# Optimization experiments

Hardware: AMD Instinct MI355X
Metric: run time of the kernel (lower is better)

Reference implementation:

```python
import jax, jax.numpy as jnp
import numpy as np

N_NODES = 100000
N_EDGES = 1600000
D_IN, D_HID, D_OUT = 128, 128, 64


def setup_inputs() -> dict:
    key = jax.random.key(0)
    ks = jax.random.split(key, 8)
    x = jax.random.normal(ks[0], (N_NODES, D_IN), dtype=jnp.float32)
    edge_index = jax.random.randint(ks[1], (2, N_EDGES), 0, N_NODES, dtype=jnp.int64)
    def glorot(k, fan_in, fan_out):
        s = jnp.sqrt(6.0 / (fan_in + fan_out))
        return jax.random.uniform(k, (fan_in, fan_out), jnp.float32, -s, s)
    return {
        "x": x,
        "edge_index": edge_index,
        "W1": glorot(ks[2], D_IN, D_HID), "b1": jnp.zeros((D_HID,), jnp.float32),
        "W2": glorot(ks[3], D_HID, D_HID), "b2": jnp.zeros((D_HID,), jnp.float32),
        "W3": glorot(ks[4], D_HID, D_OUT), "b3": jnp.zeros((D_OUT,), jnp.float32),
    }


def _gcn_norm(edge_index, n_nodes):
    # add self-loops, compute symmetric normalization D^-1/2 A D^-1/2
    loop = jnp.arange(n_nodes, dtype=edge_index.dtype)
    src = jnp.concatenate([edge_index[0], loop])  # message source
    dst = jnp.concatenate([edge_index[1], loop])  # aggregation target
    deg = jax.ops.segment_sum(jnp.ones_like(dst, dtype=jnp.float32), dst,
                              num_segments=n_nodes)
    dinv = jnp.where(deg > 0, jax.lax.rsqrt(deg), 0.0)
    norm = dinv[src] * dinv[dst]  # [E + N]
    return src, dst, norm


def _gcn_conv(x, W, b, src, dst, norm, n_nodes):
    xw = x @ W                                # dense transform [N, F_out]
    msg = xw[src] * norm[:, None]             # gather + scale   [E+N, F_out]
    out = jax.ops.segment_sum(msg, dst, num_segments=n_nodes)  # scatter-add
    return out + b


def reference(x, edge_index, W1, b1, W2, b2, W3, b3):
    n = x.shape[0]
    src, dst, norm = _gcn_norm(edge_index, n)  # cached=True: same norm reused
    h = jax.nn.relu(_gcn_conv(x, W1, b1, src, dst, norm, n))
    h = jax.nn.relu(_gcn_conv(h, W2, b2, src, dst, norm, n))
    return _gcn_conv(h, W3, b3, src, dst, norm, n)
```

## Files before the change

### kernel.cpp

```cpp
#include <hip/hip_runtime.h>
#include <hip/hip_fp16.h>


#define NN 100000
#define NE 1600000
#define TT (NE + NN)
#define BSH 9
#define NBUCK ((NN + 511) / 512)
#define EPB1 8192
#define NPB1 ((TT + EPB1 - 1) / EPB1)
#define SLOT 12288

typedef _Float16 f16x8 __attribute__((ext_vector_type(8)));
typedef float f32x4 __attribute__((ext_vector_type(4)));


__global__ __launch_bounds__(256) void wt_conv_all(const float* __restrict__ W1,
                                                   const float* __restrict__ W2,
                                                   const float* __restrict__ W3,
                                                   _Float16* __restrict__ Wt1,
                                                   _Float16* __restrict__ Wt2,
                                                   _Float16* __restrict__ Wt3,
                                                   int* __restrict__ gcursor,
                                                   int* __restrict__ rowptr) {
    int idx = blockIdx.x * 256 + threadIdx.x;
    if (idx < 16384) {
        Wt1[(idx % 128) * 128 + idx / 128] = (_Float16)W1[idx];
    } else if (idx < 32768) {
        int i = idx - 16384;
        Wt2[(i % 128) * 128 + i / 128] = (_Float16)W2[i];
    } else if (idx < 40960) {
        int i = idx - 32768;
        Wt3[(i % 64) * 128 + i / 64] = (_Float16)W3[i];
    }
    if (idx < NBUCK) gcursor[idx] = 0;
    if (idx == 0) rowptr[NN] = TT;
}


__global__ __launch_bounds__(1024) void partition_p1(const int* __restrict__ ei,
                                                     int* __restrict__ gcursor,
                                                     int* __restrict__ part) {
    __shared__ int hist[NBUCK];
    const int tid = threadIdx.x;
    const int base = blockIdx.x * EPB1;
    for (int b = tid; b < NBUCK; b += 1024) hist[b] = 0;
    __syncthreads();
    for (int i = tid; i < EPB1; i += 1024) {
        int e = base + i;
        if (e >= TT) break;
        int d = (e < NE) ? ei[NE + e] : (e - NE);
        atomicAdd(&hist[d >> BSH], 1);
    }
    __syncthreads();
    for (int b = tid; b < NBUCK; b += 1024) {
        int cnt = hist[b];
        hist[b] = cnt ? atomicAdd(&gcursor[b], cnt) : 0;
    }
    __syncthreads();
    for (int i = tid; i < EPB1; i += 1024) {
        int e = base + i;
        if (e >= TT) break;
        int s, d;
        if (e < NE) { s = ei[e]; d = ei[NE + e]; }
        else        { s = d = e - NE; }
        int bk = d >> BSH;
        int pos = atomicAdd(&hist[bk], 1);
        part[bk * SLOT + pos] = s | ((d & 511) << 17);
    }
}


__global__ __launch_bounds__(512) void partition_p2(const int* __restrict__ part,
                                                    const int* __restrict__ gcnt,
                                                    int* __restrict__ rowptr,
                                                    float* __restrict__ dinv,
                                                    int* __restrict__ col) {
    __shared__ int red[512];
    __shared__ int cnt[512];
    __shared__ int scn[512];
    __shared__ int cur[512];
    __shared__ int sbase;
    const int b = blockIdx.x;
    const int v0 = b << BSH;
    const int nv = min(512, NN - v0);
    const int tid = threadIdx.x;
    const int nrec = gcnt[b];
    const int* bp = part + (size_t)b * SLOT;

    red[tid] = (tid < b) ? gcnt[tid] : 0;
    cnt[tid] = 0;
    __syncthreads();
    for (int off = 256; off > 0; off >>= 1) {
        if (tid < off) red[tid] += red[tid + off];
        __syncthreads();
    }
    if (tid == 0) sbase = red[0];

    for (int i = tid; i < nrec; i += 512)
        atomicAdd(&cnt[((unsigned)bp[i]) >> 17], 1);
    __syncthreads();
    const int base = sbase;
    scn[tid] = cnt[tid];
    __syncthreads();
    for (int off = 1; off < 512; off <<= 1) {
        int a = (tid >= off) ? scn[tid - off] : 0;
        __syncthreads();
        scn[tid] += a;
        __syncthreads();
    }
    if (tid < nv) {
        int excl = scn[tid] - cnt[tid];
        rowptr[v0 + tid] = base + excl;
        dinv[v0 + tid] = rsqrtf((float)cnt[tid]);
        cur[tid] = base + excl;
    }
    __syncthreads();
    for (int i = tid; i < nrec; i += 512) {
        int r = bp[i];
        int pos = atomicAdd(&cur[((unsigned)r) >> 17], 1);
        col[pos] = r & 0x1FFFF;
    }
}


template <int F, bool AHALF>
__global__ __launch_bounds__(256) void gemm_mfma(const void* __restrict__ Ap,
                                                 const _Float16* __restrict__ Wt,
                                                 const float* __restrict__ dinv,
                                                 __half* __restrict__ Yh) {
    constexpr int NT = F / 16;
    __shared__ _Float16 Yl[64][136];

    const int tid = threadIdx.x;
    const int wave = tid >> 6;
    const int lane = tid & 63;
    const int m = lane & 15;
    const int q = lane >> 4;
    const int grow0 = blockIdx.x * 64;
    const int row = grow0 + wave * 16 + m;
    const bool rok = row < NN;

    f32x4 acc[NT];
#pragma unroll
    for (int t = 0; t < NT; t++) acc[t] = (f32x4){0.f, 0.f, 0.f, 0.f};

#pragma unroll
    for (int kt = 0; kt < 128; kt += 32) {
        const int k0 = kt + q * 8;
        union { f16x8 v; _Float16 e[8]; } au;
        if (rok) {
            if constexpr (AHALF) {
                au.v = *reinterpret_cast<const f16x8*>(
                    (const __half*)Ap + (size_t)row * 128 + k0);
            } else {
                const float* A = (const float*)Ap;
                float4 x0 = *reinterpret_cast<const float4*>(A + (size_t)row * 128 + k0);
                float4 x1 = *reinterpret_cast<const float4*>(A + (size_t)row * 128 + k0 + 4);
                au.e[0] = (_Float16)x0.x; au.e[1] = (_Float16)x0.y;
                au.e[2] = (_Float16)x0.z; au.e[3] = (_Float16)x0.w;
                au.e[4] = (_Float16)x1.x; au.e[5] = (_Float16)x1.y;
                au.e[6] = (_Float16)x1.z; au.e[7] = (_Float16)x1.w;
            }
        } else {
#pragma unroll
            for (int j = 0; j < 8; j++) au.e[j] = (_Float16)0.f;
        }
#pragma unroll
        for (int t = 0; t < NT; t++) {
            f16x8 bf = *reinterpret_cast<const f16x8*>(Wt + (t * 16 + m) * 128 + k0);
            acc[t] = __builtin_amdgcn_mfma_f32_16x16x32_f16(au.v, bf, acc[t], 0, 0, 0);
        }
    }
#pragma unroll
    for (int r = 0; r < 4; r++) {
        int lrow = wave * 16 + q * 4 + r;
        int gr = grow0 + lrow;
        float s = (gr < NN) ? dinv[gr] : 0.f;
#pragma unroll
        for (int t = 0; t < NT; t++)
            Yl[lrow][t * 16 + m] = (_Float16)(s * acc[t][r]);
    }
    __syncthreads();
    constexpr int CH = F / 8;
    for (int i = tid; i < 64 * CH; i += 256) {
        int lrow = i / CH, c = i % CH;
        int gr = grow0 + lrow;
        if (gr < NN)
            *reinterpret_cast<f16x8*>(Yh + (size_t)gr * F + c * 8) =
                *reinterpret_cast<const f16x8*>(&Yl[lrow][c * 8]);
    }
}


__device__ __forceinline__ void acc_add8(float* acc, float4 raw) {
    const __half2* h2 = reinterpret_cast<const __half2*>(&raw);
#pragma unroll
    for (int qq = 0; qq < 4; qq++) {
        float2 fv = __half22float2(h2[qq]);
        acc[2 * qq]     += fv.x;
        acc[2 * qq + 1] += fv.y;
    }
}


template <int FOUT>
__global__ __launch_bounds__(256) void fused_agg_gemm(
        const __half* __restrict__ XWh,
        const int* __restrict__ rowptr,
        const int* __restrict__ col,
        const float* __restrict__ dinv,
        const float* __restrict__ bias,
        const _Float16* __restrict__ Wt,
        __half* __restrict__ Yout) {
    __shared__ _Float16 Hs[16][136];
    __shared__ _Float16 Ds[16][FOUT + 8];

    const int tid = threadIdx.x;
    const int v0 = blockIdx.x * 16;

    {
        const int lnode = tid >> 4;
        const int f = tid & 15;
        const int v = v0 + lnode;
        const int beg = rowptr[v];
        const int end = rowptr[v + 1];
        const float4* base = reinterpret_cast<const float4*>(XWh);
        float acc[8] = {0.f, 0.f, 0.f, 0.f, 0.f, 0.f, 0.f, 0.f};
#pragma unroll 4
        for (int e = beg; e < end; e++) {
            int u = col[e];
            float4 raw = base[(size_t)u * 16 + f];
            acc_add8(acc, raw);
        }
        const float dv = dinv[v];
        union { f16x8 v8; _Float16 e8[8]; } hu;
#pragma unroll
        for (int qq = 0; qq < 8; qq++) {
            float r = dv * acc[qq] + bias[f * 8 + qq];
            hu.e8[qq] = (_Float16)fmaxf(r, 0.f);
        }
        *reinterpret_cast<f16x8*>(&Hs[lnode][f * 8]) = hu.v8;
    }
    __syncthreads();

    constexpr int TPW = FOUT / 64;
    const int wave = tid >> 6;
    const int lane = tid & 63;
    const int m = lane & 15;
    const int q = lane >> 4;
    f32x4 gacc[TPW];
#pragma unroll
    for (int t = 0; t < TPW; t++) gacc[t] = (f32x4){0.f, 0.f, 0.f, 0.f};
#pragma unroll
    for (int kt = 0; kt < 128; kt += 32) {
        const int k0 = kt + q * 8;
        f16x8 av = *reinterpret_cast<const f16x8*>(&Hs[m][k0]);
#pragma unroll
        for (int t = 0; t < TPW; t++) {
            const int gc = (wave * TPW + t) * 16 + m;
            f16x8 bv = *reinterpret_cast<const f16x8*>(Wt + gc * 128 + k0);
            gacc[t] = __builtin_amdgcn_mfma_f32_16x16x32_f16(av, bv, gacc[t], 0, 0, 0);
        }
    }
#pragma unroll
    for (int r = 0; r < 4; r++) {
        const int lrow = q * 4 + r;
        const float s = dinv[v0 + lrow];
#pragma unroll
        for (int t = 0; t < TPW; t++)
            Ds[lrow][(wave * TPW + t) * 16 + m] = (_Float16)(s * gacc[t][r]);
    }
    __syncthreads();
    constexpr int CH = FOUT / 8;
    for (int i2 = tid; i2 < 16 * CH; i2 += 256) {
        int lrow = i2 / CH, c = i2 % CH;
        *reinterpret_cast<f16x8*>(Yout + (size_t)(v0 + lrow) * FOUT + c * 8) =
            *reinterpret_cast<const f16x8*>(&Ds[lrow][c * 8]);
    }
}


__global__ __launch_bounds__(256) void agg_final(
        const __half* __restrict__ XWh,
        const int* __restrict__ rowptr,
        const int* __restrict__ col,
        const float* __restrict__ dinv,
        const float* __restrict__ bias,
        float* __restrict__ out) {
    constexpr int TPN = 8;
    constexpr int NPB = 256 / TPN;
    const int v = blockIdx.x * NPB + threadIdx.x / TPN;
    const int f = threadIdx.x % TPN;
    const int beg = rowptr[v];
    const int end = rowptr[v + 1];
    const float4* base = reinterpret_cast<const float4*>(XWh);
    float acc[8] = {0.f, 0.f, 0.f, 0.f, 0.f, 0.f, 0.f, 0.f};
#pragma unroll 4
    for (int e = beg; e < end; e++) {
        int u = col[e];
        float4 raw = base[(size_t)u * TPN + f];
        acc_add8(acc, raw);
    }
    const float dv = dinv[v];
    float r[8];
#pragma unroll
    for (int q = 0; q < 8; q++)
        r[q] = dv * acc[q] + bias[f * 8 + q];
    float* op = out + (size_t)v * 64 + f * 8;
    *reinterpret_cast<float4*>(op)     = make_float4(r[0], r[1], r[2], r[3]);
    *reinterpret_cast<float4*>(op + 4) = make_float4(r[4], r[5], r[6], r[7]);
}


extern "C" void kernel_launch(void* const* d_in, const int* in_sizes, int n_in,
                              void* d_out, int out_size, void* d_ws, size_t ws_size,
                              hipStream_t stream) {
    const float* x  = (const float*)d_in[0];
    const int*   ei = (const int*)d_in[1];
    const float* W1 = (const float*)d_in[2];
    const float* b1 = (const float*)d_in[3];
    const float* W2 = (const float*)d_in[4];
    const float* b2 = (const float*)d_in[5];
    const float* W3 = (const float*)d_in[6];
    const float* b3 = (const float*)d_in[7];
    float* out = (float*)d_out;

    char* p = (char*)d_ws;
    int*      rowptr  = (int*)p;       p += 400016;
    float*    dinv    = (float*)p;     p += 400000;
    int*      gcursor = (int*)p;       p += 1024;
    _Float16* Wt1     = (_Float16*)p;  p += 32768;
    _Float16* Wt2     = (_Float16*)p;  p += 32768;
    _Float16* Wt3     = (_Float16*)p;  p += 16384;
    int*      part    = (int*)p;       p += (size_t)NBUCK * SLOT * 4;
    int*      col     = (int*)p;       p += (size_t)TT * 4;
    __half*   xwh1    = (__half*)p;    p += (size_t)NN * 128 * 2;
    __half*   xwh2    = (__half*)p;
    __half*   xwh3    = xwh1;

    wt_conv_all<<<160, 256, 0, stream>>>(W1, W2, W3, Wt1, Wt2, Wt3,
                                         gcursor, rowptr);
    partition_p1<<<NPB1, 1024, 0, stream>>>(ei, gcursor, part);
    partition_p2<<<NBUCK, 512, 0, stream>>>(part, gcursor, rowptr, dinv, col);

    const int gb = (NN + 63) / 64;
    const int fb = NN / 16;
    gemm_mfma<128, false><<<gb, 256, 0, stream>>>(x, Wt1, dinv, xwh1);
    fused_agg_gemm<128><<<fb, 256, 0, stream>>>(xwh1, rowptr, col, dinv, b1,
                                                Wt2, xwh2);
    fused_agg_gemm<64><<<fb, 256, 0, stream>>>(xwh2, rowptr, col, dinv, b2,
                                               Wt3, xwh3);
    agg_final<<<NN / 32, 256, 0, stream>>>(xwh3, rowptr, col, dinv, b3, out);
}
```

Measured before the change: 399.4 us.

## Merge all stages into one persistent cooperative kernel with grid syncs

Replaces the seven separate launches (weight convert, two partition passes, GEMM, two fused agg+GEMM, final aggregation) with a single cooperative persistent kernel. Stages are separated by grid.sync and each runs as a grid-stride loop over the old block indices. Shared memory is a union of the per-stage layouts, and the fused phases process two 16-node tiles per 512-thread block. The aim is to remove launch gaps and tail effects between stages, at the cost of grid-sync overhead, fewer resident blocks (capped at 768), and a direct strided store in the first GEMM where the old code staged output through LDS.

```diff
diff --git a/kernel.cpp b/kernel.cpp
--- a/kernel.cpp
+++ b/kernel.cpp
@@ -1,5 +1,8 @@
 #include <hip/hip_runtime.h>
 #include <hip/hip_fp16.h>
+#include <hip/hip_cooperative_groups.h>
+
+namespace cg = cooperative_groups;
 
 
 #define NN 100000
@@ -7,309 +10,291 @@
 #define TT (NE + NN)
 #define BSH 9
 #define NBUCK ((NN + 511) / 512)
-#define EPB1 8192
+#define EPB1 4096
 #define NPB1 ((TT + EPB1 - 1) / EPB1)
 #define SLOT 12288
+#define GRID_BLOCKS 768
 
 typedef _Float16 f16x8 __attribute__((ext_vector_type(8)));
 typedef float f32x4 __attribute__((ext_vector_type(4)));
 
-
-__global__ __launch_bounds__(256) void wt_conv_all(const float* __restrict__ W1,
-                                                   const float* __restrict__ W2,
-                                                   const float* __restrict__ W3,
-                                                   _Float16* __restrict__ Wt1,
-                                                   _Float16* __restrict__ Wt2,
-                                                   _Float16* __restrict__ Wt3,
-                                                   int* __restrict__ gcursor,
-                                                   int* __restrict__ rowptr) {
-    int idx = blockIdx.x * 256 + threadIdx.x;
-    if (idx < 16384) {
-        Wt1[(idx % 128) * 128 + idx / 128] = (_Float16)W1[idx];
-    } else if (idx < 32768) {
-        int i = idx - 16384;
-        Wt2[(i % 128) * 128 + i / 128] = (_Float16)W2[i];
-    } else if (idx < 40960) {
-        int i = idx - 32768;
-        Wt3[(i % 64) * 128 + i / 64] = (_Float16)W3[i];
-    }
-    if (idx < NBUCK) gcursor[idx] = 0;
-    if (idx == 0) rowptr[NN] = TT;
+struct HotS { _Float16 Hs[2][16][136]; _Float16 Ds[2][16][136]; };
+struct P2S  { int red[512]; int cnt[512]; int scn[512]; int cur[512]; int sbase; };
+union SMU {
+    int  hist[NBUCK];
+    P2S  p2;
+    HotS hot;
+};
+
+__device__ __forceinline__ void acc_add8(float* acc, float4 raw) {
+    const __half2* h2 = reinterpret_cast<const __half2*>(&raw);
+#pragma unroll
+    for (int qq = 0; qq < 4; qq++) {
+        float2 fv = __half22float2(h2[qq]);
+        acc[2 * qq]     += fv.x;
+        acc[2 * qq + 1] += fv.y;
+    }
 }
 
 
-__global__ __launch_bounds__(1024) void partition_p1(const int* __restrict__ ei,
-                                                     int* __restrict__ gcursor,
-                                                     int* __restrict__ part) {
-    __shared__ int hist[NBUCK];
+template <int FOUT>
+__device__ void fused_phase(SMU& sm,
+                            const __half* __restrict__ XWh,
+                            const int* __restrict__ rowptr,
+                            const int* __restrict__ col,
+                            const float* __restrict__ dinv,
+                            const float* __restrict__ bias,
+                            const _Float16* __restrict__ Wt,
+                            __half* __restrict__ Yout) {
+    const int tid  = threadIdx.x;
+    const int half = tid >> 8;
+    const int t256 = tid & 255;
+    const int gsz  = gridDim.x;
+    for (int tb = blockIdx.x; tb < NN / 32; tb += gsz) {
+        const int v0 = (tb * 2 + half) * 16;
+        __syncthreads();
+        {
+            const int lnode = t256 >> 4;
+            const int f = t256 & 15;
+            const int v = v0 + lnode;
+            const int beg = rowptr[v];
+            const int end = rowptr[v + 1];
+            const float4* base = reinterpret_cast<const float4*>(XWh);
+            float acc[8] = {0.f, 0.f, 0.f, 0.f, 0.f, 0.f, 0.f, 0.f};
+#pragma unroll 4
+            for (int e = beg; e < end; e++) {
+                int u = col[e];
+                float4 raw = base[(size_t)u * 16 + f];
+                acc_add8(acc, raw);
+            }
+            const float dv = dinv[v];
+            union { f16x8 v8; _Float16 e8[8]; } hu;
+#pragma unroll
+            for (int qq = 0; qq < 8; qq++) {
+                float r = dv * acc[qq] + bias[f * 8 + qq];
+                hu.e8[qq] = (_Float16)fmaxf(r, 0.f);
+            }
+            *reinterpret_cast<f16x8*>(&sm.hot.Hs[half][lnode][f * 8]) = hu.v8;
+        }
+        __syncthreads();
+        constexpr int TPW = FOUT / 64;
+        const int wave = t256 >> 6;
+        const int lane = t256 & 63;
+        const int m = lane & 15;
+        const int q = lane >> 4;
+        f32x4 gacc[TPW];
+#pragma unroll
+        for (int t = 0; t < TPW; t++) gacc[t] = (f32x4){0.f, 0.f, 0.f, 0.f};
+#pragma unroll
+        for (int kt = 0; kt < 128; kt += 32) {
+            const int k0 = kt + q * 8;
+            f16x8 av = *reinterpret_cast<const f16x8*>(&sm.hot.Hs[half][m][k0]);
+#pragma unroll
+            for (int t = 0; t < TPW; t++) {
+                const int gc = (wave * TPW + t) * 16 + m;
+                f16x8 bv = *reinterpret_cast<const f16x8*>(Wt + gc * 128 + k0);
+                gacc[t] = __builtin_amdgcn_mfma_f32_16x16x32_f16(av, bv, gacc[t], 0, 0, 0);
+            }
+        }
+#pragma unroll
+        for (int r = 0; r < 4; r++) {
+            const int lrow = q * 4 + r;
+            const float s = dinv[v0 + lrow];
+#pragma unroll
+            for (int t = 0; t < TPW; t++)
+                sm.hot.Ds[half][lrow][(wave * TPW + t) * 16 + m] =
+                    (_Float16)(s * gacc[t][r]);
+        }
+        __syncthreads();
+        constexpr int CH = FOUT / 8;
+        for (int i2 = t256; i2 < 16 * CH; i2 += 256) {
+            int lrow = i2 / CH, c = i2 % CH;
+            *reinterpret_cast<f16x8*>(Yout + (size_t)(v0 + lrow) * FOUT + c * 8) =
+                *reinterpret_cast<const f16x8*>(&sm.hot.Ds[half][lrow][c * 8]);
+        }
+    }
+}
+
+
+__global__ __launch_bounds__(512, 6) void mega(
+        const float* __restrict__ x, const int* __restrict__ ei,
+        const float* __restrict__ W1, const float* __restrict__ b1,
+        const float* __restrict__ W2, const float* __restrict__ b2,
+        const float* __restrict__ W3, const float* __restrict__ b3,
+        _Float16* __restrict__ Wt1, _Float16* __restrict__ Wt2,
+        _Float16* __restrict__ Wt3,
+        int* __restrict__ gcursor, int* __restrict__ rowptr,
+        float* __restrict__ dinv, int* __restrict__ part,
+        int* __restrict__ col,
+        __half* __restrict__ xwh1, __half* __restrict__ xwh2,
+        float* __restrict__ out) {
+    cg::grid_group grid = cg::this_grid();
+    __shared__ SMU sm;
     const int tid = threadIdx.x;
-    const int base = blockIdx.x * EPB1;
-    for (int b = tid; b < NBUCK; b += 1024) hist[b] = 0;
-    __syncthreads();
-    for (int i = tid; i < EPB1; i += 1024) {
-        int e = base + i;
-        if (e >= TT) break;
-        int d = (e < NE) ? ei[NE + e] : (e - NE);
-        atomicAdd(&hist[d >> BSH], 1);
-    }
-    __syncthreads();
-    for (int b = tid; b < NBUCK; b += 1024) {
-        int cnt = hist[b];
-        hist[b] = cnt ? atomicAdd(&gcursor[b], cnt) : 0;
-    }
-    __syncthreads();
-    for (int i = tid; i < EPB1; i += 1024) {
-        int e = base + i;
-        if (e >= TT) break;
-        int s, d;
-        if (e < NE) { s = ei[e]; d = ei[NE + e]; }
-        else        { s = d = e - NE; }
-        int bk = d >> BSH;
-        int pos = atomicAdd(&hist[bk], 1);
-        part[bk * SLOT + pos] = s | ((d & 511) << 17);
-    }
-}
-
-
-__global__ __launch_bounds__(512) void partition_p2(const int* __restrict__ part,
-                                                    const int* __restrict__ gcnt,
-                                                    int* __restrict__ rowptr,
-                                                    float* __restrict__ dinv,
-                                                    int* __restrict__ col) {
-    __shared__ int red[512];
-    __shared__ int cnt[512];
-    __shared__ int scn[512];
-    __shared__ int cur[512];
-    __shared__ int sbase;
-    const int b = blockIdx.x;
-    const int v0 = b << BSH;
-    const int nv = min(512, NN - v0);
-    const int tid = threadIdx.x;
-    const int nrec = gcnt[b];
-    const int* bp = part + (size_t)b * SLOT;
-
-    red[tid] = (tid < b) ? gcnt[tid] : 0;
-    cnt[tid] = 0;
-    __syncthreads();
-    for (int off = 256; off > 0; off >>= 1) {
-        if (tid < off) red[tid] += red[tid + off];
-        __syncthreads();
-    }
-    if (tid == 0) sbase = red[0];
-
-    for (int i = tid; i < nrec; i += 512)
-        atomicAdd(&cnt[((unsigned)bp[i]) >> 17], 1);
-    __syncthreads();
-    const int base = sbase;
-    scn[tid] = cnt[tid];
-    __syncthreads();
-    for (int off = 1; off < 512; off <<= 1) {
-        int a = (tid >= off) ? scn[tid - off] : 0;
-        __syncthreads();
-        scn[tid] += a;
-        __syncthreads();
-    }
-    if (tid < nv) {
-        int excl = scn[tid] - cnt[tid];
-        rowptr[v0 + tid] = base + excl;
-        dinv[v0 + tid] = rsqrtf((float)cnt[tid]);
-        cur[tid] = base + excl;
-    }
-    __syncthreads();
-    for (int i = tid; i < nrec; i += 512) {
-        int r = bp[i];
-        int pos = atomicAdd(&cur[((unsigned)r) >> 17], 1);
-        col[pos] = r & 0x1FFFF;
-    }
-}
-
-
-template <int F, bool AHALF>
-__global__ __launch_bounds__(256) void gemm_mfma(const void* __restrict__ Ap,
-                                                 const _Float16* __restrict__ Wt,
-                                                 const float* __restrict__ dinv,
-                                                 __half* __restrict__ Yh) {
-    constexpr int NT = F / 16;
-    __shared__ _Float16 Yl[64][136];
-
-    const int tid = threadIdx.x;
-    const int wave = tid >> 6;
-    const int lane = tid & 63;
-    const int m = lane & 15;
-    const int q = lane >> 4;
-    const int grow0 = blockIdx.x * 64;
-    const int row = grow0 + wave * 16 + m;
-    const bool rok = row < NN;
-
-    f32x4 acc[NT];
-#pragma unroll
-    for (int t = 0; t < NT; t++) acc[t] = (f32x4){0.f, 0.f, 0.f, 0.f};
-
-#pragma unroll
-    for (int kt = 0; kt < 128; kt += 32) {
-        const int k0 = kt + q * 8;
-        union { f16x8 v; _Float16 e[8]; } au;
-        if (rok) {
-            if constexpr (AHALF) {
-                au.v = *reinterpret_cast<const f16x8*>(
-                    (const __half*)Ap + (size_t)row * 128 + k0);
-            } else {
-                const float* A = (const float*)Ap;
-                float4 x0 = *reinterpret_cast<const float4*>(A + (size_t)row * 128 + k0);
-                float4 x1 = *reinterpret_cast<const float4*>(A + (size_t)row * 128 + k0 + 4);
+    const int gsz = gridDim.x;
+
+    {
+        int idx = blockIdx.x * 512 + tid;
+        if (idx < 16384) {
+            Wt1[(idx % 128) * 128 + idx / 128] = (_Float16)W1[idx];
+        } else if (idx < 32768) {
+            int i = idx - 16384;
+            Wt2[(i % 128) * 128 + i / 128] = (_Float16)W2[i];
+        } else if (idx < 40960) {
+            int i = idx - 32768;
+            Wt3[(i % 64) * 128 + i / 64] = (_Float16)W3[i];
+        }
+        if (idx < NBUCK) gcursor[idx] = 0;
+        if (idx == 0) rowptr[NN] = TT;
+    }
+    grid.sync();
+
+    for (int c = blockIdx.x; c < NPB1; c += gsz) {
+        __syncthreads();
+        for (int b = tid; b < NBUCK; b += 512) sm.hist[b] = 0;
+        __syncthreads();
+        const int base = c * EPB1;
+        for (int i = tid; i < EPB1; i += 512) {
+            int e = base + i;
+            if (e >= TT) break;
+            int d = (e < NE) ? ei[NE + e] : (e - NE);
+            atomicAdd(&sm.hist[d >> BSH], 1);
+        }
+        __syncthreads();
+        for (int b = tid; b < NBUCK; b += 512) {
+            int cnt = sm.hist[b];
+            sm.hist[b] = cnt ? atomicAdd(&gcursor[b], cnt) : 0;
+        }
+        __syncthreads();
+        for (int i = tid; i < EPB1; i += 512) {
+            int e = base + i;
+            if (e >= TT) break;
+            int s, d;
+            if (e < NE) { s = ei[e]; d = ei[NE + e]; }
+            else        { s = d = e - NE; }
+            int bk = d >> BSH;
+            int pos = atomicAdd(&sm.hist[bk], 1);
+            part[bk * SLOT + pos] = s | ((d & 511) << 17);
+        }
+    }
+    grid.sync();
+
+    for (int b = blockIdx.x; b < NBUCK; b += gsz) {
+        const int v0 = b << BSH;
+        const int nv = min(512, NN - v0);
+        const int nrec = gcursor[b];
+        const int* bp = part + (size_t)b * SLOT;
+        sm.p2.red[tid] = (tid < b) ? gcursor[tid] : 0;
+        sm.p2.cnt[tid] = 0;
+        __syncthreads();
+        for (int off = 256; off > 0; off >>= 1) {
+            if (tid < off) sm.p2.red[tid] += sm.p2.red[tid + off];
+            __syncthreads();
+        }
+        if (tid == 0) sm.p2.sbase = sm.p2.red[0];
+        for (int i = tid; i < nrec; i += 512)
+            atomicAdd(&sm.p2.cnt[((unsigned)bp[i]) >> 17], 1);
+        __syncthreads();
+        const int base = sm.p2.sbase;
+        sm.p2.scn[tid] = sm.p2.cnt[tid];
+        __syncthreads();
+        for (int off = 1; off < 512; off <<= 1) {
+            int a = (tid >= off) ? sm.p2.scn[tid - off] : 0;
+            __syncthreads();
+            sm.p2.scn[tid] += a;
+            __syncthreads();
+        }
+        if (tid < nv) {
+            int excl = sm.p2.scn[tid] - sm.p2.cnt[tid];
+            rowptr[v0 + tid] = base + excl;
+            dinv[v0 + tid] = rsqrtf((float)sm.p2.cnt[tid]);
+            sm.p2.cur[tid] = base + excl;
+        }
+        __syncthreads();
+        for (int i = tid; i < nrec; i += 512) {
+            int r = bp[i];
+            int pos = atomicAdd(&sm.p2.cur[((unsigned)r) >> 17], 1);
+            col[pos] = r & 0x1FFFF;
+        }
+    }
+    grid.sync();
+
+    for (int tb = blockIdx.x; tb < (NN + 127) / 128; tb += gsz) {
+        const int wave = tid >> 6;
+        const int lane = tid & 63;
+        const int m = lane & 15;
+        const int q = lane >> 4;
+        const int grow0 = tb * 128;
+        const int row = grow0 + wave * 16 + m;
+        const bool rok = row < NN;
+        f32x4 acc[8];
+#pragma unroll
+        for (int t = 0; t < 8; t++) acc[t] = (f32x4){0.f, 0.f, 0.f, 0.f};
+#pragma unroll
+        for (int kt = 0; kt < 128; kt += 32) {
+            const int k0 = kt + q * 8;
+            union { f16x8 v; _Float16 e[8]; } au;
+            if (rok) {
+                float4 x0 = *reinterpret_cast<const float4*>(x + (size_t)row * 128 + k0);
+                float4 x1 = *reinterpret_cast<const float4*>(x + (size_t)row * 128 + k0 + 4);
                 au.e[0] = (_Float16)x0.x; au.e[1] = (_Float16)x0.y;
                 au.e[2] = (_Float16)x0.z; au.e[3] = (_Float16)x0.w;
                 au.e[4] = (_Float16)x1.x; au.e[5] = (_Float16)x1.y;
                 au.e[6] = (_Float16)x1.z; au.e[7] = (_Float16)x1.w;
-            }
-        } else {
-#pragma unroll
-            for (int j = 0; j < 8; j++) au.e[j] = (_Float16)0.f;
-        }
-#pragma unroll
-        for (int t = 0; t < NT; t++) {
-            f16x8 bf = *reinterpret_cast<const f16x8*>(Wt + (t * 16 + m) * 128 + k0);
-            acc[t] = __builtin_amdgcn_mfma_f32_16x16x32_f16(au.v, bf, acc[t], 0, 0, 0);
-        }
-    }
-#pragma unroll
-    for (int r = 0; r < 4; r++) {
-        int lrow = wave * 16 + q * 4 + r;
-        int gr = grow0 + lrow;
-        float s = (gr < NN) ? dinv[gr] : 0.f;
-#pragma unroll
-        for (int t = 0; t < NT; t++)
-            Yl[lrow][t * 16 + m] = (_Float16)(s * acc[t][r]);
-    }
-    __syncthreads();
-    constexpr int CH = F / 8;
-    for (int i = tid; i < 64 * CH; i += 256) {
-        int lrow = i / CH, c = i % CH;
-        int gr = grow0 + lrow;
-        if (gr < NN)
-            *reinterpret_cast<f16x8*>(Yh + (size_t)gr * F + c * 8) =
-                *reinterpret_cast<const f16x8*>(&Yl[lrow][c * 8]);
-    }
-}
-
-
-__device__ __forceinline__ void acc_add8(float* acc, float4 raw) {
-    const __half2* h2 = reinterpret_cast<const __half2*>(&raw);
-#pragma unroll
-    for (int qq = 0; qq < 4; qq++) {
-        float2 fv = __half22float2(h2[qq]);
-        acc[2 * qq]     += fv.x;
-        acc[2 * qq + 1] += fv.y;
-    }
-}
-
-
-template <int FOUT>
-__global__ __launch_bounds__(256) void fused_agg_gemm(
-        const __half* __restrict__ XWh,
-        const int* __restrict__ rowptr,
-        const int* __restrict__ col,
-        const float* __restrict__ dinv,
-        const float* __restrict__ bias,
-        const _Float16* __restrict__ Wt,
-        __half* __restrict__ Yout) {
-    __shared__ _Float16 Hs[16][136];
-    __shared__ _Float16 Ds[16][FOUT + 8];
-
-    const int tid = threadIdx.x;
-    const int v0 = blockIdx.x * 16;
-
-    {
-        const int lnode = tid >> 4;
-        const int f = tid & 15;
-        const int v = v0 + lnode;
-        const int beg = rowptr[v];
-        const int end = rowptr[v + 1];
-        const float4* base = reinterpret_cast<const float4*>(XWh);
-        float acc[8] = {0.f, 0.f, 0.f, 0.f, 0.f, 0.f, 0.f, 0.f};
+            } else {
+#pragma unroll
+                for (int j = 0; j < 8; j++) au.e[j] = (_Float16)0.f;
+            }
+#pragma unroll
+            for (int t = 0; t < 8; t++) {
+                f16x8 bf = *reinterpret_cast<const f16x8*>(Wt1 + (t * 16 + m) * 128 + k0);
+                acc[t] = __builtin_amdgcn_mfma_f32_16x16x32_f16(au.v, bf, acc[t], 0, 0, 0);
+            }
+        }
+        _Float16* Y = reinterpret_cast<_Float16*>(xwh1);
+#pragma unroll
+        for (int r = 0; r < 4; r++) {
+            int gr = grow0 + wave * 16 + q * 4 + r;
+            if (gr < NN) {
+                float s = dinv[gr];
+#pragma unroll
+                for (int t = 0; t < 8; t++)
+                    Y[(size_t)gr * 128 + t * 16 + m] = (_Float16)(s * acc[t][r]);
+            }
+        }
+    }
+    grid.sync();
+
+    fused_phase<128>(sm, xwh1, rowptr, col, dinv, b1, Wt2, xwh2);
+    grid.sync();
+
+    fused_phase<64>(sm, xwh2, rowptr, col, dinv, b2, Wt3, xwh1);
+    grid.sync();
+
+    for (int tb = blockIdx.x; tb < (NN + 63) / 64; tb += gsz) {
+        const int v = tb * 64 + (tid >> 3);
+        const int f = tid & 7;
+        if (v < NN) {
+            const int beg = rowptr[v];
+            const int end = rowptr[v + 1];
+            const float4* base = reinterpret_cast<const float4*>(xwh1);
+            float acc[8] = {0.f, 0.f, 0.f, 0.f, 0.f, 0.f, 0.f, 0.f};
 #pragma unroll 4
-        for (int e = beg; e < end; e++) {
-            int u = col[e];
-            float4 raw = base[(size_t)u * 16 + f];
-            acc_add8(acc, raw);
-        }
-        const float dv = dinv[v];
-        union { f16x8 v8; _Float16 e8[8]; } hu;
-#pragma unroll
-        for (int qq = 0; qq < 8; qq++) {
-            float r = dv * acc[qq] + bias[f * 8 + qq];
-            hu.e8[qq] = (_Float16)fmaxf(r, 0.f);
-        }
-        *reinterpret_cast<f16x8*>(&Hs[lnode][f * 8]) = hu.v8;
-    }
-    __syncthreads();
-
-    constexpr int TPW = FOUT / 64;
-    const int wave = tid >> 6;
-    const int lane = tid & 63;
-    const int m = lane & 15;
-    const int q = lane >> 4;
-    f32x4 gacc[TPW];
-#pragma unroll
-    for (int t = 0; t < TPW; t++) gacc[t] = (f32x4){0.f, 0.f, 0.f, 0.f};
-#pragma unroll
-    for (int kt = 0; kt < 128; kt += 32) {
-        const int k0 = kt + q * 8;
-        f16x8 av = *reinterpret_cast<const f16x8*>(&Hs[m][k0]);
-#pragma unroll
-        for (int t = 0; t < TPW; t++) {
-            const int gc = (wave * TPW + t) * 16 + m;
-            f16x8 bv = *reinterpret_cast<const f16x8*>(Wt + gc * 128 + k0);
-            gacc[t] = __builtin_amdgcn_mfma_f32_16x16x32_f16(av, bv, gacc[t], 0, 0, 0);
-        }
-    }
-#pragma unroll
-    for (int r = 0; r < 4; r++) {
-        const int lrow = q * 4 + r;
-        const float s = dinv[v0 + lrow];
-#pragma unroll
-        for (int t = 0; t < TPW; t++)
-            Ds[lrow][(wave * TPW + t) * 16 + m] = (_Float16)(s * gacc[t][r]);
-    }
-    __syncthreads();
-    constexpr int CH = FOUT / 8;
-    for (int i2 = tid; i2 < 16 * CH; i2 += 256) {
-        int lrow = i2 / CH, c = i2 % CH;
-        *reinterpret_cast<f16x8*>(Yout + (size_t)(v0 + lrow) * FOUT + c * 8) =
-            *reinterpret_cast<const f16x8*>(&Ds[lrow][c * 8]);
-    }
-}
-
-
-__global__ __launch_bounds__(256) void agg_final(
-        const __half* __restrict__ XWh,
-        const int* __restrict__ rowptr,
-        const int* __restrict__ col,
-        const float* __restrict__ dinv,
-        const float* __restrict__ bias,
-        float* __restrict__ out) {
-    constexpr int TPN = 8;
-    constexpr int NPB = 256 / TPN;
-    const int v = blockIdx.x * NPB + threadIdx.x / TPN;
-    const int f = threadIdx.x % TPN;
-    const int beg = rowptr[v];
-    const int end = rowptr[v + 1];
-    const float4* base = reinterpret_cast<const float4*>(XWh);
-    float acc[8] = {0.f, 0.f, 0.f, 0.f, 0.f, 0.f, 0.f, 0.f};
-#pragma unroll 4
-    for (int e = beg; e < end; e++) {
-        int u = col[e];
-        float4 raw = base[(size_t)u * TPN + f];
-        acc_add8(acc, raw);
-    }
-    const float dv = dinv[v];
-    float r[8];
-#pragma unroll
-    for (int q = 0; q < 8; q++)
-        r[q] = dv * acc[q] + bias[f * 8 + q];
-    float* op = out + (size_t)v * 64 + f * 8;
-    *reinterpret_cast<float4*>(op)     = make_float4(r[0], r[1], r[2], r[3]);
-    *reinterpret_cast<float4*>(op + 4) = make_float4(r[4], r[5], r[6], r[7]);
+            for (int e = beg; e < end; e++) {
+                int u = col[e];
+                float4 raw = base[(size_t)u * 8 + f];
+                acc_add8(acc, raw);
+            }
+            const float dv = dinv[v];
+            float r[8];
+#pragma unroll
+            for (int qq = 0; qq < 8; qq++)
+                r[qq] = dv * acc[qq] + b3[f * 8 + qq];
+            float* op = out + (size_t)v * 64 + f * 8;
+            *reinterpret_cast<float4*>(op)     = make_float4(r[0], r[1], r[2], r[3]);
+            *reinterpret_cast<float4*>(op + 4) = make_float4(r[4], r[5], r[6], r[7]);
+        }
+    }
 }
 
 
@@ -337,19 +322,26 @@
     int*      col     = (int*)p;       p += (size_t)TT * 4;
     __half*   xwh1    = (__half*)p;    p += (size_t)NN * 128 * 2;
     __half*   xwh2    = (__half*)p;
-    __half*   xwh3    = xwh1;
-
-    wt_conv_all<<<160, 256, 0, stream>>>(W1, W2, W3, Wt1, Wt2, Wt3,
-                                         gcursor, rowptr);
-    partition_p1<<<NPB1, 1024, 0, stream>>>(ei, gcursor, part);
-    partition_p2<<<NBUCK, 512, 0, stream>>>(part, gcursor, rowptr, dinv, col);
-
-    const int gb = (NN + 63) / 64;
-    const int fb = NN / 16;
-    gemm_mfma<128, false><<<gb, 256, 0, stream>>>(x, Wt1, dinv, xwh1);
-    fused_agg_gemm<128><<<fb, 256, 0, stream>>>(xwh1, rowptr, col, dinv, b1,
-                                                Wt2, xwh2);
-    fused_agg_gemm<64><<<fb, 256, 0, stream>>>(xwh2, rowptr, col, dinv, b2,
-                                               Wt3, xwh3);
-    agg_final<<<NN / 32, 256, 0, stream>>>(xwh3, rowptr, col, dinv, b3, out);
+
+    static int s_grid = 0;
+    if (s_grid == 0) {
+        hipDeviceProp_t prop;
+        hipGetDeviceProperties(&prop, 0);
+        int nb = 0;
+        hipOccupancyMaxActiveBlocksPerMultiprocessor(&nb, (const void*)mega, 512, 0);
+        if (nb < 1) nb = 1;
+        long g = (long)nb * prop.multiProcessorCount;
+        if (g > GRID_BLOCKS) g = GRID_BLOCKS;
+        s_grid = (int)g;
+    }
+
+    void* args[] = {(void*)&x, (void*)&ei,
+                    (void*)&W1, (void*)&b1, (void*)&W2, (void*)&b2,
+                    (void*)&W3, (void*)&b3,
+                    (void*)&Wt1, (void*)&Wt2, (void*)&Wt3,
+                    (void*)&gcursor, (void*)&rowptr, (void*)&dinv,
+                    (void*)&part, (void*)&col,
+                    (void*)&xwh1, (void*)&xwh2, (void*)&out};
+    hipLaunchCooperativeKernel((void*)mega, dim3(s_grid), dim3(512),
+                               args, 0, stream);
 }
```

Result: slower. 743.4 us (+86.1%).

## Fuse CSR partition second pass with first-layer GEMM in one kernel

Applied to the files above, without the earlier changes.

Merges the per-bucket CSR build kernel with the first-layer MFMA GEMM. Each 1024-thread block builds the rows for its 512 nodes, keeps their dinv in shared memory, then computes x·W1 for those rows in two 256-row passes. This removes a kernel launch and the global dinv reread. The cost is that the GEMM now runs on only one block per bucket (about 196 large blocks), which lowers parallelism and latency hiding, and the LDS footprint grows.

```diff
diff --git a/kernel.cpp b/kernel.cpp
--- a/kernel.cpp
+++ b/kernel.cpp
@@ -71,16 +71,22 @@
 }
 
 
-__global__ __launch_bounds__(512) void partition_p2(const int* __restrict__ part,
-                                                    const int* __restrict__ gcnt,
-                                                    int* __restrict__ rowptr,
-                                                    float* __restrict__ dinv,
-                                                    int* __restrict__ col) {
+__global__ __launch_bounds__(1024) void partition_gemm(
+        const int* __restrict__ part,
+        const int* __restrict__ gcnt,
+        const float* __restrict__ x,
+        const _Float16* __restrict__ Wt1,
+        int* __restrict__ rowptr,
+        float* __restrict__ dinv,
+        int* __restrict__ col,
+        __half* __restrict__ xwh1) {
     __shared__ int red[512];
     __shared__ int cnt[512];
     __shared__ int scn[512];
     __shared__ int cur[512];
-    __shared__ int sbase;
+    __shared__ float sdinv[512];
+    __shared__ _Float16 Yl[256][136];
+    __shared__ int sbase_s;
     const int b = blockIdx.x;
     const int v0 = b << BSH;
     const int nv = min(512, NN - v0);
@@ -88,107 +94,95 @@
     const int nrec = gcnt[b];
     const int* bp = part + (size_t)b * SLOT;
 
-    red[tid] = (tid < b) ? gcnt[tid] : 0;
-    cnt[tid] = 0;
+    if (tid < 512) { red[tid] = (tid < b) ? gcnt[tid] : 0; cnt[tid] = 0; }
     __syncthreads();
     for (int off = 256; off > 0; off >>= 1) {
         if (tid < off) red[tid] += red[tid + off];
         __syncthreads();
     }
-    if (tid == 0) sbase = red[0];
-
-    for (int i = tid; i < nrec; i += 512)
+    if (tid == 0) sbase_s = red[0];
+    for (int i = tid; i < nrec; i += 1024)
         atomicAdd(&cnt[((unsigned)bp[i]) >> 17], 1);
     __syncthreads();
-    const int base = sbase;
-    scn[tid] = cnt[tid];
+    const int base = sbase_s;
+    if (tid < 512) scn[tid] = cnt[tid];
     __syncthreads();
     for (int off = 1; off < 512; off <<= 1) {
-        int a = (tid >= off) ? scn[tid - off] : 0;
-        __syncthreads();
-        scn[tid] += a;
-        __syncthreads();
-    }
-    if (tid < nv) {
-        int excl = scn[tid] - cnt[tid];
-        rowptr[v0 + tid] = base + excl;
-        dinv[v0 + tid] = rsqrtf((float)cnt[tid]);
-        cur[tid] = base + excl;
-    }
-    __syncthreads();
-    for (int i = tid; i < nrec; i += 512) {
+        int a = (tid < 512 && tid >= off) ? scn[tid - off] : 0;
+        __syncthreads();
+        if (tid < 512) scn[tid] += a;
+        __syncthreads();
+    }
+    if (tid < 512) {
+        float dv_t = 0.f;
+        if (tid < nv) {
+            int excl = scn[tid] - cnt[tid];
+            rowptr[v0 + tid] = base + excl;
+            dv_t = rsqrtf((float)cnt[tid]);
+            dinv[v0 + tid] = dv_t;
+            cur[tid] = base + excl;
+        }
+        sdinv[tid] = dv_t;
+    }
+    __syncthreads();
+    for (int i = tid; i < nrec; i += 1024) {
         int r = bp[i];
         int pos = atomicAdd(&cur[((unsigned)r) >> 17], 1);
         col[pos] = r & 0x1FFFF;
     }
-}
-
-
-template <int F, bool AHALF>
-__global__ __launch_bounds__(256) void gemm_mfma(const void* __restrict__ Ap,
-                                                 const _Float16* __restrict__ Wt,
-                                                 const float* __restrict__ dinv,
-                                                 __half* __restrict__ Yh) {
-    constexpr int NT = F / 16;
-    __shared__ _Float16 Yl[64][136];
-
-    const int tid = threadIdx.x;
+
     const int wave = tid >> 6;
     const int lane = tid & 63;
     const int m = lane & 15;
     const int q = lane >> 4;
-    const int grow0 = blockIdx.x * 64;
-    const int row = grow0 + wave * 16 + m;
-    const bool rok = row < NN;
-
-    f32x4 acc[NT];
-#pragma unroll
-    for (int t = 0; t < NT; t++) acc[t] = (f32x4){0.f, 0.f, 0.f, 0.f};
-
-#pragma unroll
-    for (int kt = 0; kt < 128; kt += 32) {
-        const int k0 = kt + q * 8;
-        union { f16x8 v; _Float16 e[8]; } au;
-        if (rok) {
-            if constexpr (AHALF) {
-                au.v = *reinterpret_cast<const f16x8*>(
-                    (const __half*)Ap + (size_t)row * 128 + k0);
-            } else {
-                const float* A = (const float*)Ap;
-                float4 x0 = *reinterpret_cast<const float4*>(A + (size_t)row * 128 + k0);
-                float4 x1 = *reinterpret_cast<const float4*>(A + (size_t)row * 128 + k0 + 4);
+#pragma unroll 1
+    for (int pass = 0; pass < 2; pass++) {
+        const int rb = pass * 256;
+        const int lr0 = wave * 16;
+        const int j = rb + lr0 + m;
+        const int row = v0 + j;
+        const bool rok = j < nv;
+        f32x4 acc[8];
+#pragma unroll
+        for (int t = 0; t < 8; t++) acc[t] = (f32x4){0.f, 0.f, 0.f, 0.f};
+#pragma unroll
+        for (int kt = 0; kt < 128; kt += 32) {
+            const int k0 = kt + q * 8;
+            union { f16x8 v; _Float16 e[8]; } au;
+            if (rok) {
+                float4 x0 = *reinterpret_cast<const float4*>(x + (size_t)row * 128 + k0);
+                float4 x1 = *reinterpret_cast<const float4*>(x + (size_t)row * 128 + k0 + 4);
                 au.e[0] = (_Float16)x0.x; au.e[1] = (_Float16)x0.y;
                 au.e[2] = (_Float16)x0.z; au.e[3] = (_Float16)x0.w;
                 au.e[4] = (_Float16)x1.x; au.e[5] = (_Float16)x1.y;
                 au.e[6] = (_Float16)x1.z; au.e[7] = (_Float16)x1.w;
+            } else {
+#pragma unroll
+                for (int jj = 0; jj < 8; jj++) au.e[jj] = (_Float16)0.f;
             }
-        } else {
-#pragma unroll
-            for (int j = 0; j < 8; j++) au.e[j] = (_Float16)0.f;
-        }
-#pragma unroll
-        for (int t = 0; t < NT; t++) {
-            f16x8 bf = *reinterpret_cast<const f16x8*>(Wt + (t * 16 + m) * 128 + k0);
-            acc[t] = __builtin_amdgcn_mfma_f32_16x16x32_f16(au.v, bf, acc[t], 0, 0, 0);
-        }
-    }
-#pragma unroll
-    for (int r = 0; r < 4; r++) {
-        int lrow = wave * 16 + q * 4 + r;
-        int gr = grow0 + lrow;
-        float s = (gr < NN) ? dinv[gr] : 0.f;
-#pragma unroll
-        for (int t = 0; t < NT; t++)
-            Yl[lrow][t * 16 + m] = (_Float16)(s * acc[t][r]);
-    }
-    __syncthreads();
-    constexpr int CH = F / 8;
-    for (int i = tid; i < 64 * CH; i += 256) {
-        int lrow = i / CH, c = i % CH;
-        int gr = grow0 + lrow;
-        if (gr < NN)
-            *reinterpret_cast<f16x8*>(Yh + (size_t)gr * F + c * 8) =
-                *reinterpret_cast<const f16x8*>(&Yl[lrow][c * 8]);
+#pragma unroll
+            for (int t = 0; t < 8; t++) {
+                f16x8 bf = *reinterpret_cast<const f16x8*>(Wt1 + (t * 16 + m) * 128 + k0);
+                acc[t] = __builtin_amdgcn_mfma_f32_16x16x32_f16(au.v, bf, acc[t], 0, 0, 0);
+            }
+        }
+#pragma unroll
+        for (int r = 0; r < 4; r++) {
+            const int lr = lr0 + q * 4 + r;
+            const float s = sdinv[rb + lr];
+#pragma unroll
+            for (int t = 0; t < 8; t++)
+                Yl[lr][t * 16 + m] = (_Float16)(s * acc[t][r]);
+        }
+        __syncthreads();
+        for (int i2 = tid; i2 < 256 * 16; i2 += 1024) {
+            int lr = i2 >> 4, c = i2 & 15;
+            int jj = rb + lr;
+            if (jj < nv)
+                *reinterpret_cast<f16x8*>(xwh1 + (size_t)(v0 + jj) * 128 + c * 8) =
+                    *reinterpret_cast<const f16x8*>(&Yl[lr][c * 8]);
+        }
+        __syncthreads();
     }
 }
 
@@ -342,11 +336,10 @@
     wt_conv_all<<<160, 256, 0, stream>>>(W1, W2, W3, Wt1, Wt2, Wt3,
                                          gcursor, rowptr);
     partition_p1<<<NPB1, 1024, 0, stream>>>(ei, gcursor, part);
-    partition_p2<<<NBUCK, 512, 0, stream>>>(part, gcursor, rowptr, dinv, col);
-
-    const int gb = (NN + 63) / 64;
+    partition_gemm<<<NBUCK, 1024, 0, stream>>>(part, gcursor, x, Wt1,
+                                               rowptr, dinv, col, xwh1);
+
     const int fb = NN / 16;
-    gemm_mfma<128, false><<<gb, 256, 0, stream>>>(x, Wt1, dinv, xwh1);
     fused_agg_gemm<128><<<fb, 256, 0, stream>>>(xwh1, rowptr, col, dinv, b1,
                                                 Wt2, xwh2);
     fused_agg_gemm<64><<<fb, 256, 0, stream>>>(xwh2, rowptr, col, dinv, b2,
```

New measurement: 436.9 us. +9.4%, slower.

## Split GEMM outputs into feature-slice layout and unfuse aggregation from GEMM

Applied to the files above, without the earlier changes.

The GEMM now writes its output as eight contiguous feature slices, one per 16 (or 8) columns, instead of row-major. Aggregation kernels assign one block column to each slice, so the random neighbour gathers in any interleaved group of blocks touch a much smaller working set and hit L2 more often. The fused aggregate+GEMM kernels are replaced by separate aggregation and GEMM launches, which costs an extra round trip of the hidden activations through memory and more launches. Each edge's column index is also re-read once per slice.

```diff
diff --git a/kernel.cpp b/kernel.cpp
--- a/kernel.cpp
+++ b/kernel.cpp
@@ -183,12 +183,17 @@
     }
     __syncthreads();
     constexpr int CH = F / 8;
+    constexpr int CPS = CH / 8;
+    constexpr int SF = F / 8;
     for (int i = tid; i < 64 * CH; i += 256) {
         int lrow = i / CH, c = i % CH;
         int gr = grow0 + lrow;
-        if (gr < NN)
-            *reinterpret_cast<f16x8*>(Yh + (size_t)gr * F + c * 8) =
+        if (gr < NN) {
+            int sl = c / CPS, w = c % CPS;
+            *reinterpret_cast<f16x8*>(
+                Yh + (size_t)sl * NN * SF + (size_t)gr * SF + w * 8) =
                 *reinterpret_cast<const f16x8*>(&Yl[lrow][c * 8]);
+        }
     }
 }
 
@@ -204,110 +209,69 @@
 }
 
 
-template <int FOUT>
-__global__ __launch_bounds__(256) void fused_agg_gemm(
-        const __half* __restrict__ XWh,
+__global__ __launch_bounds__(256) void agg_slice128(
+        const __half* __restrict__ XWs,
         const int* __restrict__ rowptr,
         const int* __restrict__ col,
         const float* __restrict__ dinv,
         const float* __restrict__ bias,
-        const _Float16* __restrict__ Wt,
-        __half* __restrict__ Yout) {
-    __shared__ _Float16 Hs[16][136];
-    __shared__ _Float16 Ds[16][FOUT + 8];
-
+        __half* __restrict__ Hout) {
+    const int s = blockIdx.x & 7;
+    const int g = blockIdx.x >> 3;
     const int tid = threadIdx.x;
-    const int v0 = blockIdx.x * 16;
-
-    {
-        const int lnode = tid >> 4;
-        const int f = tid & 15;
-        const int v = v0 + lnode;
-        const int beg = rowptr[v];
-        const int end = rowptr[v + 1];
-        const float4* base = reinterpret_cast<const float4*>(XWh);
-        float acc[8] = {0.f, 0.f, 0.f, 0.f, 0.f, 0.f, 0.f, 0.f};
+    const int lnode = tid >> 1;
+    const int half = tid & 1;
+    const int v = g * 128 + lnode;
+    if (v >= NN) return;
+    const int beg = rowptr[v];
+    const int end = rowptr[v + 1];
+    const float4* sbase = reinterpret_cast<const float4*>(XWs + (size_t)s * NN * 16);
+    float acc[8] = {0.f, 0.f, 0.f, 0.f, 0.f, 0.f, 0.f, 0.f};
 #pragma unroll 4
-        for (int e = beg; e < end; e++) {
-            int u = col[e];
-            float4 raw = base[(size_t)u * 16 + f];
-            acc_add8(acc, raw);
-        }
-        const float dv = dinv[v];
-        union { f16x8 v8; _Float16 e8[8]; } hu;
-#pragma unroll
-        for (int qq = 0; qq < 8; qq++) {
-            float r = dv * acc[qq] + bias[f * 8 + qq];
-            hu.e8[qq] = (_Float16)fmaxf(r, 0.f);
-        }
-        *reinterpret_cast<f16x8*>(&Hs[lnode][f * 8]) = hu.v8;
-    }
-    __syncthreads();
-
-    constexpr int TPW = FOUT / 64;
-    const int wave = tid >> 6;
-    const int lane = tid & 63;
-    const int m = lane & 15;
-    const int q = lane >> 4;
-    f32x4 gacc[TPW];
-#pragma unroll
-    for (int t = 0; t < TPW; t++) gacc[t] = (f32x4){0.f, 0.f, 0.f, 0.f};
-#pragma unroll
-    for (int kt = 0; kt < 128; kt += 32) {
-        const int k0 = kt + q * 8;
-        f16x8 av = *reinterpret_cast<const f16x8*>(&Hs[m][k0]);
-#pragma unroll
-        for (int t = 0; t < TPW; t++) {
-            const int gc = (wave * TPW + t) * 16 + m;
-            f16x8 bv = *reinterpret_cast<const f16x8*>(Wt + gc * 128 + k0);
-            gacc[t] = __builtin_amdgcn_mfma_f32_16x16x32_f16(av, bv, gacc[t], 0, 0, 0);
-        }
-    }
-#pragma unroll
-    for (int r = 0; r < 4; r++) {
-        const int lrow = q * 4 + r;
-        const float s = dinv[v0 + lrow];
-#pragma unroll
-        for (int t = 0; t < TPW; t++)
-            Ds[lrow][(wave * TPW + t) * 16 + m] = (_Float16)(s * gacc[t][r]);
-    }
-    __syncthreads();
-    constexpr int CH = FOUT / 8;
-    for (int i2 = tid; i2 < 16 * CH; i2 += 256) {
-        int lrow = i2 / CH, c = i2 % CH;
-        *reinterpret_cast<f16x8*>(Yout + (size_t)(v0 + lrow) * FOUT + c * 8) =
-            *reinterpret_cast<const f16x8*>(&Ds[lrow][c * 8]);
-    }
-}
-
-
-__global__ __launch_bounds__(256) void agg_final(
-        const __half* __restrict__ XWh,
+    for (int e = beg; e < end; e++) {
+        int u = col[e];
+        float4 raw = sbase[u * 2 + half];
+        acc_add8(acc, raw);
+    }
+    const float dv = dinv[v];
+    const int f0 = s * 16 + half * 8;
+    union { f16x8 v8; _Float16 e8[8]; } hu;
+#pragma unroll
+    for (int qq = 0; qq < 8; qq++) {
+        float r = dv * acc[qq] + bias[f0 + qq];
+        hu.e8[qq] = (_Float16)fmaxf(r, 0.f);
+    }
+    *reinterpret_cast<f16x8*>(Hout + (size_t)v * 128 + f0) = hu.v8;
+}
+
+
+__global__ __launch_bounds__(256) void agg_final_slice(
+        const __half* __restrict__ XWs,
         const int* __restrict__ rowptr,
         const int* __restrict__ col,
         const float* __restrict__ dinv,
         const float* __restrict__ bias,
         float* __restrict__ out) {
-    constexpr int TPN = 8;
-    constexpr int NPB = 256 / TPN;
-    const int v = blockIdx.x * NPB + threadIdx.x / TPN;
-    const int f = threadIdx.x % TPN;
+    const int s = blockIdx.x & 7;
+    const int g = blockIdx.x >> 3;
+    const int v = g * 256 + threadIdx.x;
+    if (v >= NN) return;
     const int beg = rowptr[v];
     const int end = rowptr[v + 1];
-    const float4* base = reinterpret_cast<const float4*>(XWh);
+    const float4* sbase = reinterpret_cast<const float4*>(XWs + (size_t)s * NN * 8);
     float acc[8] = {0.f, 0.f, 0.f, 0.f, 0.f, 0.f, 0.f, 0.f};
 #pragma unroll 4
     for (int e = beg; e < end; e++) {
         int u = col[e];
-        float4 raw = base[(size_t)u * TPN + f];
+        float4 raw = sbase[u];
         acc_add8(acc, raw);
     }
     const float dv = dinv[v];
     float r[8];
 #pragma unroll
-    for (int q = 0; q < 8; q++)
-        r[q] = dv * acc[q] + bias[f * 8 + q];
-    float* op = out + (size_t)v * 64 + f * 8;
+    for (int qq = 0; qq < 8; qq++)
+        r[qq] = dv * acc[qq] + bias[s * 8 + qq];
+    float* op = out + (size_t)v * 64 + s * 8;
     *reinterpret_cast<float4*>(op)     = make_float4(r[0], r[1], r[2], r[3]);
     *reinterpret_cast<float4*>(op + 4) = make_float4(r[4], r[5], r[6], r[7]);
 }
@@ -335,9 +299,8 @@
     _Float16* Wt3     = (_Float16*)p;  p += 16384;
     int*      part    = (int*)p;       p += (size_t)NBUCK * SLOT * 4;
     int*      col     = (int*)p;       p += (size_t)TT * 4;
-    __half*   xwh1    = (__half*)p;    p += (size_t)NN * 128 * 2;
-    __half*   xwh2    = (__half*)p;
-    __half*   xwh3    = xwh1;
+    __half*   bufA    = (__half*)p;    p += (size_t)NN * 128 * 2;
+    __half*   bufB    = (__half*)p;
 
     wt_conv_all<<<160, 256, 0, stream>>>(W1, W2, W3, Wt1, Wt2, Wt3,
                                          gcursor, rowptr);
@@ -345,11 +308,13 @@
     partition_p2<<<NBUCK, 512, 0, stream>>>(part, gcursor, rowptr, dinv, col);
 
     const int gb = (NN + 63) / 64;
-    const int fb = NN / 16;
-    gemm_mfma<128, false><<<gb, 256, 0, stream>>>(x, Wt1, dinv, xwh1);
-    fused_agg_gemm<128><<<fb, 256, 0, stream>>>(xwh1, rowptr, col, dinv, b1,
-                                                Wt2, xwh2);
-    fused_agg_gemm<64><<<fb, 256, 0, stream>>>(xwh2, rowptr, col, dinv, b2,
-                                               Wt3, xwh3);
-    agg_final<<<NN / 32, 256, 0, stream>>>(xwh3, rowptr, col, dinv, b3, out);
-}
+    const int ga128 = ((NN + 127) / 128) * 8;
+    const int gaf   = ((NN + 255) / 256) * 8;
+
+    gemm_mfma<128, false><<<gb, 256, 0, stream>>>(x, Wt1, dinv, bufA);
+    agg_slice128<<<ga128, 256, 0, stream>>>(bufA, rowptr, col, dinv, b1, bufB);
+    gemm_mfma<128, true><<<gb, 256, 0, stream>>>(bufB, Wt2, dinv, bufA);
+    agg_slice128<<<ga128, 256, 0, stream>>>(bufA, rowptr, col, dinv, b2, bufB);
+    gemm_mfma<64, true><<<gb, 256, 0, stream>>>(bufB, Wt3, dinv, bufA);
+    agg_final_slice<<<gaf, 256, 0, stream>>>(bufA, rowptr, col, dinv, b3, out);
+}
```

Result: slower. 540.5 us (+35.3%).
